# Kernel optimization log

Measured on AMD Instinct MI355X. Metric: run time of the kernel, lower is better.

## Reference

```python
import jax, jax.numpy as jnp
import numpy as np

T, B, H, V, L = 1024, 16, 1024, 100, 3


def setup_inputs() -> dict:
    key = jax.random.key(0)
    k_x, k_e, k_w, k_b = jax.random.split(key, 4)
    x = jax.random.randint(k_x, (T, B), 0, V)                      # [T, B] token ids
    emb = jax.random.normal(k_e, (V, H), dtype=jnp.float32) * 0.1  # embedding table
    # per-layer Linear(H, 3H): stacked weights/biases (all layers have in=out=H)
    W = jax.random.normal(k_w, (L, H, 3 * H), dtype=jnp.float32) * (1.0 / np.sqrt(H))
    b = jax.random.normal(k_b, (L, 3 * H), dtype=jnp.float32) * 0.01
    return {"x": x, "emb": emb, "W": W, "b": b}


def _qrnn_layer(h, W_l, b_l):
    # h: [T, B, H] -> gates [T, B, 3H]
    g = jnp.einsum("tbh,hk->tbk", h, W_l) + b_l
    z, f, o = jnp.split(g, 3, axis=-1)
    z = jnp.tanh(z)
    f = jax.nn.sigmoid(f)
    o = jax.nn.sigmoid(o)

    def step(c, zf):
        z_t, f_t = zf
        c = f_t * z_t + (1.0 - f_t) * c  # forget-mult recurrence
        return c, c

    c0 = jnp.zeros(h.shape[1:], dtype=h.dtype)  # hidden init is None -> zeros
    _, C = jax.lax.scan(step, c0, (z, f))       # C: [T, B, H]
    return o * C


def reference(x, emb, W, b):
    h = emb[x]  # [T, B, H]
    for l in range(L):
        h = _qrnn_layer(h, W[l], b[l])
    return h[:-1]  # drop last timestep, [T-1, B, H]
```

## Files before the change

### kernel.cpp

```cpp
#include <hip/hip_runtime.h>
#include <hip/hip_bf16.h>

#define T_DIM 1024
#define B_DIM 16
#define H_DIM 1024
#define L_DIM 3
#define M_DIM (T_DIM * B_DIM)
#define N_DIM (3 * H_DIM)
#define K_DIM H_DIM
#define NC 64
#define CS 16

typedef __bf16 bf16x8 __attribute__((ext_vector_type(8)));
typedef __bf16 bf16x4 __attribute__((ext_vector_type(4)));
typedef _Float16 half4 __attribute__((ext_vector_type(4)));
typedef float f32x4 __attribute__((ext_vector_type(4)));

__device__ __forceinline__ __bf16 f2bf(float f) {
    return (__bf16)__float2bfloat16(f);
}

__device__ __forceinline__ void async_cp16(const void* g, void* lds) {
    __builtin_amdgcn_global_load_lds(
        (__attribute__((address_space(1))) void*)g,
        (__attribute__((address_space(3))) void*)lds, 16, 0, 0);
}

#define TW_BLOCKS (32 * 96 * 3)
__global__ void prep_kernel(const float* __restrict__ W, __bf16* __restrict__ Wt,
                            const int* __restrict__ x, const float4* __restrict__ emb,
                            __bf16* __restrict__ h) {
    if (blockIdx.x < TW_BLOCKS) {
        __shared__ __bf16 tile[32][33];
        const int blk = blockIdx.x;
        const int l = blk / 3072;
        const int r2 = blk % 3072;
        const int n0 = (r2 / 32) * 32, k0 = (r2 % 32) * 32;
        const int tx = threadIdx.x & 31, ty = threadIdx.x >> 5;
        const float* Wl = W + (size_t)l * K_DIM * N_DIM;
        __bf16* Wtl = Wt + (size_t)l * N_DIM * K_DIM;
#pragma unroll
        for (int q = 0; q < 4; q++) {
            int k = ty + q * 8;
            tile[k][tx] = f2bf(Wl[(size_t)(k0 + k) * N_DIM + n0 + tx]);
        }
        __syncthreads();
#pragma unroll
        for (int q = 0; q < 4; q++) {
            int n = ty + q * 8;
            Wtl[(size_t)(n0 + n) * K_DIM + k0 + tx] = tile[tx][n];
        }
    } else {
        int i = (blockIdx.x - TW_BLOCKS) * 256 + threadIdx.x;
        int row = i >> 8;
        int j = i & 255;
        int idx = x[row];
        float4 v = emb[(size_t)idx * 256 + j];
        __bf16* dst = h + (size_t)row * H_DIM + j * 4;
        dst[0] = f2bf(v.x); dst[1] = f2bf(v.y); dst[2] = f2bf(v.z); dst[3] = f2bf(v.w);
    }
}

__global__ __launch_bounds__(512, 2) void gemm_gates(
    const __bf16* __restrict__ A,
    const __bf16* __restrict__ Wt,
    const float* __restrict__ bias,
    _Float16* __restrict__ Gz, _Float16* __restrict__ Gf, _Float16* __restrict__ Go) {
    __shared__ __align__(16) __bf16 As[4 * 8192];
    __shared__ __align__(16) __bf16 Bs[4 * 8192];

    const int tid = threadIdx.x;
    const int lane = tid & 63, wid = tid >> 6;
    const int lm = lane & 15, kg = lane >> 4;
    const int waveM = wid >> 2, waveN = wid & 3;

    const int orig = blockIdx.x;
    const int lin = (orig & 7) * 96 + (orig >> 3);
    const int bm = lin / 12, bn = lin % 12;

    const int sr = tid >> 2;
    const int sch = (tid & 3) ^ ((sr >> 1) & 3);
    const int ga0 = sr * K_DIM + sch * 8;
    const int ga1 = (sr + 128) * K_DIM + sch * 8;
    const int lo0 = tid * 8;
    const int lo1 = (512 + tid) * 8;

    const __bf16* Abase = A + (size_t)(bm * 256) * K_DIM;
    const __bf16* Bbase = Wt + (size_t)(bn * 256) * K_DIM;

    const int slot8 = (kg ^ ((lm >> 1) & 3)) * 8;
    const int a_off0 = (waveM * 128 + 0 * 16 + lm) * 32 + slot8;
    const int a_off1 = (waveM * 128 + 1 * 16 + lm) * 32 + slot8;
    const int a_off2 = (waveM * 128 + 2 * 16 + lm) * 32 + slot8;
    const int a_off3 = (waveM * 128 + 3 * 16 + lm) * 32 + slot8;
    const int b_off0 = (waveN * 64 + 0 * 16 + lm) * 32 + slot8;
    const int b_off1 = (waveN * 64 + 1 * 16 + lm) * 32 + slot8;
    const int b_off2 = (waveN * 64 + 2 * 16 + lm) * 32 + slot8;
    const int b_off3 = (waveN * 64 + 3 * 16 + lm) * 32 + slot8;

    f32x4 acc[8][4] = {};
    bf16x8 af0, af1, af2, af3;
    bf16x8 bf0 = {}, bf1 = {}, bf2 = {}, bf3 = {};

#define STAGE(ARR, GB, TILE, KH) { \
    const int tt_ = (TILE) & 15; \
    const int kc_ = tt_ * 64 + (KH) * 32; \
    __bf16* dst_ = (ARR) + ((tt_ & 1) * 2 + (KH)) * 8192; \
    async_cp16((GB) + kc_ + ga0, dst_ + lo0); \
    async_cp16((GB) + kc_ + ga1, dst_ + lo1); }

#define MF1(IA, J, AF, BF) \
    acc[IA][J] = __builtin_amdgcn_mfma_f32_16x16x32_bf16(AF, BF, acc[IA][J], 0, 0, 0);
#define MF4(IA, AF) MF1(IA, 0, AF, bf0) MF1(IA, 1, AF, bf1) MF1(IA, 2, AF, bf2) MF1(IA, 3, AF, bf3)

#define PHASE(BUF, KH, MQ, LB, STG, VM) { \
    const __bf16* rA_ = As + ((BUF) * 2 + (KH)) * 8192 + (MQ) * 2048; \
    if (LB) { \
        const __bf16* rB_ = Bs + ((BUF) * 2 + (KH)) * 8192; \
        bf0 = *(const bf16x8*)(rB_ + b_off0); \
        bf1 = *(const bf16x8*)(rB_ + b_off1); \
        bf2 = *(const bf16x8*)(rB_ + b_off2); \
        bf3 = *(const bf16x8*)(rB_ + b_off3); } \
    af0 = *(const bf16x8*)(rA_ + a_off0); \
    af1 = *(const bf16x8*)(rA_ + a_off1); \
    af2 = *(const bf16x8*)(rA_ + a_off2); \
    af3 = *(const bf16x8*)(rA_ + a_off3); \
    STG; \
    __builtin_amdgcn_s_setprio(1); \
    MF4((MQ) * 4 + 0, af0) MF4((MQ) * 4 + 1, af1) MF4((MQ) * 4 + 2, af2) MF4((MQ) * 4 + 3, af3) \
    __builtin_amdgcn_s_setprio(0); \
    if (VM) { asm volatile("s_waitcnt vmcnt(8)" ::: "memory"); } \
    __builtin_amdgcn_s_barrier(); \
    __builtin_amdgcn_sched_barrier(0); }

    STAGE(As, Abase, 0, 0) STAGE(Bs, Bbase, 0, 0)
    STAGE(As, Abase, 0, 1) STAGE(Bs, Bbase, 0, 1)
    STAGE(As, Abase, 1, 0) STAGE(Bs, Bbase, 1, 0)
    asm volatile("s_waitcnt vmcnt(8)" ::: "memory");
    __builtin_amdgcn_s_barrier();
    __builtin_amdgcn_sched_barrier(0);

#pragma unroll 1
    for (int t = 0; t < 16; t += 2) {
        PHASE(0, 0, 0, 1, STAGE(As, Abase, t + 1, 1), 0)
        PHASE(0, 0, 1, 0, STAGE(Bs, Bbase, t + 1, 1), 1)
        PHASE(0, 1, 0, 1, STAGE(As, Abase, t + 2, 0), 0)
        PHASE(0, 1, 1, 0, STAGE(Bs, Bbase, t + 2, 0), 1)
        PHASE(1, 0, 0, 1, STAGE(As, Abase, t + 2, 1), 0)
        PHASE(1, 0, 1, 0, STAGE(Bs, Bbase, t + 2, 1), 1)
        PHASE(1, 1, 0, 1, STAGE(As, Abase, t + 3, 0), 0)
        PHASE(1, 1, 1, 0, STAGE(Bs, Bbase, t + 3, 0), 1)
    }
    asm volatile("s_waitcnt vmcnt(0)" ::: "memory");

#undef PHASE
#undef MF4
#undef MF1
#undef STAGE

    const int plane = bn >> 2;
    _Float16* __restrict__ P = (plane == 0) ? Gz : (plane == 1) ? Gf : Go;
    const int colbase = (bn & 3) * 256 + waveN * 64;
    const int nb = bn * 256 + waveN * 64;
#pragma unroll
    for (int mq = 0; mq < 2; mq++) {
#pragma unroll
        for (int i = 0; i < 4; i++) {
#pragma unroll
            for (int j = 0; j < 4; j++) {
                int col = colbase + j * 16 + lm;
                float bv = bias[nb + j * 16 + lm];
#pragma unroll
                for (int r = 0; r < 4; r++) {
                    int mrow = bm * 256 + waveM * 128 + mq * 64 + i * 16 + kg * 4 + r;
                    float g = acc[mq * 4 + i][j][r] + bv;
                    float val;
                    if (plane == 0) {
                        float e = __expf(-2.0f * fabsf(g));
                        float rc = __builtin_amdgcn_rcpf(1.0f + e);
                        val = copysignf(fmaf(-2.0f * e, rc, 1.0f), g);
                    } else {
                        float e = __expf(-g);
                        val = __builtin_amdgcn_rcpf(1.0f + e);
                    }
                    P[(size_t)mrow * H_DIM + col] = (_Float16)val;
                }
            }
        }
    }
}

__global__ __launch_bounds__(256, 8) void scan_pass1(
    const _Float16* __restrict__ Gz, const _Float16* __restrict__ Gf,
    float* __restrict__ cA, float* __restrict__ cM) {
    int tidg = blockIdx.x * 256 + threadIdx.x;
    int ci = tidg >> 12;
    int chg = tidg & 4095;
    size_t base = (size_t)(ci * CS) * 16384 + (size_t)chg * 4;
    f32x4 Aacc = {0.f, 0.f, 0.f, 0.f};
    f32x4 Macc = {1.f, 1.f, 1.f, 1.f};
#pragma unroll
    for (int s = 0; s < CS; s++) {
        half4 z = *(const half4*)(Gz + base);
        half4 f = *(const half4*)(Gf + base);
#pragma unroll
        for (int k = 0; k < 4; k++) {
            float fk = (float)f[k], zk = (float)z[k];
            Aacc[k] = fk * zk + (1.f - fk) * Aacc[k];
            Macc[k] = (1.f - fk) * Macc[k];
        }
        base += 16384;
    }
    size_t idx = (size_t)ci * 16384 + (size_t)chg * 4;
    *(f32x4*)(cA + idx) = Aacc;
    *(f32x4*)(cM + idx) = Macc;
}

__global__ __launch_bounds__(256, 8) void scan_pass23(
    const _Float16* __restrict__ Gz, const _Float16* __restrict__ Gf,
    const _Float16* __restrict__ Go,
    const float* __restrict__ cA, const float* __restrict__ cM,
    __bf16* __restrict__ hdst, float* __restrict__ fdst, int is_last) {
    int tidg = blockIdx.x * 256 + threadIdx.x;
    int ci = tidg >> 12;
    int chg = tidg & 4095;
    f32x4 c = {0.f, 0.f, 0.f, 0.f};
    for (int cj = 0; cj < ci; cj++) {
        size_t jdx = (size_t)cj * 16384 + (size_t)chg * 4;
        f32x4 a = *(const f32x4*)(cA + jdx);
        f32x4 m = *(const f32x4*)(cM + jdx);
#pragma unroll
        for (int k = 0; k < 4; k++) c[k] = a[k] + m[k] * c[k];
    }
    size_t p = (size_t)(ci * CS) * 16384 + (size_t)chg * 4;
#pragma unroll
    for (int s = 0; s < CS; s++) {
        int t = ci * CS + s;
        half4 z = *(const half4*)(Gz + p);
        half4 f = *(const half4*)(Gf + p);
        half4 o = *(const half4*)(Go + p);
        f32x4 val;
#pragma unroll
        for (int k = 0; k < 4; k++) {
            float fk = (float)f[k];
            c[k] = fk * (float)z[k] + (1.f - fk) * c[k];
            val[k] = (float)o[k] * c[k];
        }
        if (is_last) {
            if (t < T_DIM - 1)
                *(f32x4*)(fdst + p) = val;
        } else {
            bf16x4 hv;
#pragma unroll
            for (int k = 0; k < 4; k++) hv[k] = f2bf(val[k]);
            *(bf16x4*)(hdst + p) = hv;
        }
        p += 16384;
    }
}

extern "C" void kernel_launch(void* const* d_in, const int* in_sizes, int n_in,
                              void* d_out, int out_size, void* d_ws, size_t ws_size,
                              hipStream_t stream) {
    const int* x = (const int*)d_in[0];
    const float* emb = (const float*)d_in[1];
    const float* W = (const float*)d_in[2];
    const float* b = (const float*)d_in[3];
    float* out = (float*)d_out;

    char* ws = (char*)d_ws;
    size_t need = (size_t)L_DIM * N_DIM * K_DIM * 2
                + (size_t)M_DIM * H_DIM * 2
                + 3ull * M_DIM * H_DIM * 2
                + 2ull * NC * 16384 * 4;
    if (ws_size < need) return;

    __bf16* Wt = (__bf16*)ws;     ws += (size_t)L_DIM * N_DIM * K_DIM * 2;
    __bf16* hbuf = (__bf16*)ws;   ws += (size_t)M_DIM * H_DIM * 2;
    _Float16* Gz = (_Float16*)ws; ws += (size_t)M_DIM * H_DIM * 2;
    _Float16* Gf = (_Float16*)ws; ws += (size_t)M_DIM * H_DIM * 2;
    _Float16* Go = (_Float16*)ws; ws += (size_t)M_DIM * H_DIM * 2;
    float* cA = (float*)ws;       ws += (size_t)NC * 16384 * 4;
    float* cM = (float*)ws;

    prep_kernel<<<TW_BLOCKS + 16384, 256, 0, stream>>>(W, Wt, x, (const float4*)emb, hbuf);

    for (int l = 0; l < L_DIM; l++) {
        gemm_gates<<<dim3(768), 512, 0, stream>>>(
            hbuf, Wt + (size_t)l * N_DIM * K_DIM, b + (size_t)l * N_DIM, Gz, Gf, Go);
        int last = (l == L_DIM - 1);
        scan_pass1<<<1024, 256, 0, stream>>>(Gz, Gf, cA, cM);
        scan_pass23<<<1024, 256, 0, stream>>>(Gz, Gf, Go, cA, cM, hbuf, out, last);
    }
}
```

Before: 564.9 us.

## Shrink GEMM tile to 128x256 with simple double-buffered K loop for occupancy

The gate GEMM block tile is halved in M (256 to 128), so the grid doubles to 1536 blocks. LDS use drops from 128 KB to 48 KB per block and the launch bounds ask for 4 blocks per CU. The elaborate 4-buffer, 8-phase software pipeline with partial vmcnt waits is replaced by a plain two-buffer loop over 32-wide K steps, which waits on vmcnt(0) every iteration. The aim is to hide latency through occupancy rather than explicit pipelining, at the cost of lower per-block operand reuse, more barriers and less overlap of global loads with MFMA work.

```diff
diff --git a/kernel.cpp b/kernel.cpp
--- a/kernel.cpp
+++ b/kernel.cpp
@@ -61,130 +61,117 @@
     }
 }
 
-__global__ __launch_bounds__(512, 2) void gemm_gates(
+__global__ __launch_bounds__(512, 4) void gemm_gates(
     const __bf16* __restrict__ A,
     const __bf16* __restrict__ Wt,
     const float* __restrict__ bias,
     _Float16* __restrict__ Gz, _Float16* __restrict__ Gf, _Float16* __restrict__ Go) {
-    __shared__ __align__(16) __bf16 As[4 * 8192];
-    __shared__ __align__(16) __bf16 Bs[4 * 8192];
+    __shared__ __align__(16) __bf16 As[2 * 4096];
+    __shared__ __align__(16) __bf16 Bs[2 * 8192];
 
     const int tid = threadIdx.x;
     const int lane = tid & 63, wid = tid >> 6;
     const int lm = lane & 15, kg = lane >> 4;
-    const int waveM = wid >> 2, waveN = wid & 3;
+    const int wm = wid >> 2, wn = wid & 3;
 
     const int orig = blockIdx.x;
-    const int lin = (orig & 7) * 96 + (orig >> 3);
+    const int lin = (orig & 7) * 192 + (orig >> 3);
     const int bm = lin / 12, bn = lin % 12;
 
-    const int sr = tid >> 2;
-    const int sch = (tid & 3) ^ ((sr >> 1) & 3);
-    const int ga0 = sr * K_DIM + sch * 8;
-    const int ga1 = (sr + 128) * K_DIM + sch * 8;
-    const int lo0 = tid * 8;
-    const int lo1 = (512 + tid) * 8;
-
-    const __bf16* Abase = A + (size_t)(bm * 256) * K_DIM;
+    const int arow = tid >> 2;
+    const int asch = (tid & 3) ^ ((arow >> 1) & 3);
+    const int gaA = arow * K_DIM + asch * 8;
+    const int loA = tid * 8;
+    const int brow0 = tid >> 2, brow1 = (512 + tid) >> 2;
+    const int bsch0 = (tid & 3) ^ ((brow0 >> 1) & 3);
+    const int bsch1 = (tid & 3) ^ ((brow1 >> 1) & 3);
+    const int gaB0 = brow0 * K_DIM + bsch0 * 8;
+    const int gaB1 = brow1 * K_DIM + bsch1 * 8;
+    const int loB0 = tid * 8;
+    const int loB1 = (512 + tid) * 8;
+
+    const __bf16* Abase = A + (size_t)(bm * 128) * K_DIM;
     const __bf16* Bbase = Wt + (size_t)(bn * 256) * K_DIM;
 
     const int slot8 = (kg ^ ((lm >> 1) & 3)) * 8;
-    const int a_off0 = (waveM * 128 + 0 * 16 + lm) * 32 + slot8;
-    const int a_off1 = (waveM * 128 + 1 * 16 + lm) * 32 + slot8;
-    const int a_off2 = (waveM * 128 + 2 * 16 + lm) * 32 + slot8;
-    const int a_off3 = (waveM * 128 + 3 * 16 + lm) * 32 + slot8;
-    const int b_off0 = (waveN * 64 + 0 * 16 + lm) * 32 + slot8;
-    const int b_off1 = (waveN * 64 + 1 * 16 + lm) * 32 + slot8;
-    const int b_off2 = (waveN * 64 + 2 * 16 + lm) * 32 + slot8;
-    const int b_off3 = (waveN * 64 + 3 * 16 + lm) * 32 + slot8;
-
-    f32x4 acc[8][4] = {};
-    bf16x8 af0, af1, af2, af3;
-    bf16x8 bf0 = {}, bf1 = {}, bf2 = {}, bf3 = {};
-
-#define STAGE(ARR, GB, TILE, KH) { \
-    const int tt_ = (TILE) & 15; \
-    const int kc_ = tt_ * 64 + (KH) * 32; \
-    __bf16* dst_ = (ARR) + ((tt_ & 1) * 2 + (KH)) * 8192; \
-    async_cp16((GB) + kc_ + ga0, dst_ + lo0); \
-    async_cp16((GB) + kc_ + ga1, dst_ + lo1); }
-
-#define MF1(IA, J, AF, BF) \
-    acc[IA][J] = __builtin_amdgcn_mfma_f32_16x16x32_bf16(AF, BF, acc[IA][J], 0, 0, 0);
-#define MF4(IA, AF) MF1(IA, 0, AF, bf0) MF1(IA, 1, AF, bf1) MF1(IA, 2, AF, bf2) MF1(IA, 3, AF, bf3)
-
-#define PHASE(BUF, KH, MQ, LB, STG, VM) { \
-    const __bf16* rA_ = As + ((BUF) * 2 + (KH)) * 8192 + (MQ) * 2048; \
-    if (LB) { \
-        const __bf16* rB_ = Bs + ((BUF) * 2 + (KH)) * 8192; \
-        bf0 = *(const bf16x8*)(rB_ + b_off0); \
-        bf1 = *(const bf16x8*)(rB_ + b_off1); \
-        bf2 = *(const bf16x8*)(rB_ + b_off2); \
-        bf3 = *(const bf16x8*)(rB_ + b_off3); } \
-    af0 = *(const bf16x8*)(rA_ + a_off0); \
-    af1 = *(const bf16x8*)(rA_ + a_off1); \
-    af2 = *(const bf16x8*)(rA_ + a_off2); \
-    af3 = *(const bf16x8*)(rA_ + a_off3); \
-    STG; \
-    __builtin_amdgcn_s_setprio(1); \
-    MF4((MQ) * 4 + 0, af0) MF4((MQ) * 4 + 1, af1) MF4((MQ) * 4 + 2, af2) MF4((MQ) * 4 + 3, af3) \
-    __builtin_amdgcn_s_setprio(0); \
-    if (VM) { asm volatile("s_waitcnt vmcnt(8)" ::: "memory"); } \
-    __builtin_amdgcn_s_barrier(); \
-    __builtin_amdgcn_sched_barrier(0); }
-
-    STAGE(As, Abase, 0, 0) STAGE(Bs, Bbase, 0, 0)
-    STAGE(As, Abase, 0, 1) STAGE(Bs, Bbase, 0, 1)
-    STAGE(As, Abase, 1, 0) STAGE(Bs, Bbase, 1, 0)
-    asm volatile("s_waitcnt vmcnt(8)" ::: "memory");
+    const int a_off0 = (wm * 64 + 0 * 16 + lm) * 32 + slot8;
+    const int a_off1 = (wm * 64 + 1 * 16 + lm) * 32 + slot8;
+    const int a_off2 = (wm * 64 + 2 * 16 + lm) * 32 + slot8;
+    const int a_off3 = (wm * 64 + 3 * 16 + lm) * 32 + slot8;
+    const int b_off0 = (wn * 64 + 0 * 16 + lm) * 32 + slot8;
+    const int b_off1 = (wn * 64 + 1 * 16 + lm) * 32 + slot8;
+    const int b_off2 = (wn * 64 + 2 * 16 + lm) * 32 + slot8;
+    const int b_off3 = (wn * 64 + 3 * 16 + lm) * 32 + slot8;
+
+    f32x4 acc[4][4] = {};
+
+#define STAGE(TN) { \
+    const int kc_ = (TN) * 32; \
+    const int nb_ = (TN) & 1; \
+    async_cp16(Abase + kc_ + gaA, As + nb_ * 4096 + loA); \
+    async_cp16(Bbase + kc_ + gaB0, Bs + nb_ * 8192 + loB0); \
+    async_cp16(Bbase + kc_ + gaB1, Bs + nb_ * 8192 + loB1); }
+
+    STAGE(0)
+    asm volatile("s_waitcnt vmcnt(0)" ::: "memory");
     __builtin_amdgcn_s_barrier();
     __builtin_amdgcn_sched_barrier(0);
 
 #pragma unroll 1
-    for (int t = 0; t < 16; t += 2) {
-        PHASE(0, 0, 0, 1, STAGE(As, Abase, t + 1, 1), 0)
-        PHASE(0, 0, 1, 0, STAGE(Bs, Bbase, t + 1, 1), 1)
-        PHASE(0, 1, 0, 1, STAGE(As, Abase, t + 2, 0), 0)
-        PHASE(0, 1, 1, 0, STAGE(Bs, Bbase, t + 2, 0), 1)
-        PHASE(1, 0, 0, 1, STAGE(As, Abase, t + 2, 1), 0)
-        PHASE(1, 0, 1, 0, STAGE(Bs, Bbase, t + 2, 1), 1)
-        PHASE(1, 1, 0, 1, STAGE(As, Abase, t + 3, 0), 0)
-        PHASE(1, 1, 1, 0, STAGE(Bs, Bbase, t + 3, 0), 1)
-    }
-    asm volatile("s_waitcnt vmcnt(0)" ::: "memory");
-
-#undef PHASE
-#undef MF4
-#undef MF1
+    for (int t = 0; t < 32; ++t) {
+        const int cur = t & 1;
+        const __bf16* rA = As + cur * 4096;
+        const __bf16* rB = Bs + cur * 8192;
+        bf16x8 bf0 = *(const bf16x8*)(rB + b_off0);
+        bf16x8 bf1 = *(const bf16x8*)(rB + b_off1);
+        bf16x8 bf2 = *(const bf16x8*)(rB + b_off2);
+        bf16x8 bf3 = *(const bf16x8*)(rB + b_off3);
+        bf16x8 af0 = *(const bf16x8*)(rA + a_off0);
+        bf16x8 af1 = *(const bf16x8*)(rA + a_off1);
+        bf16x8 af2 = *(const bf16x8*)(rA + a_off2);
+        bf16x8 af3 = *(const bf16x8*)(rA + a_off3);
+        const int tn = (t + 1) & 31;
+        STAGE(tn)
+        __builtin_amdgcn_s_setprio(1);
+#define MFJ(I, AF) \
+        acc[I][0] = __builtin_amdgcn_mfma_f32_16x16x32_bf16(AF, bf0, acc[I][0], 0, 0, 0); \
+        acc[I][1] = __builtin_amdgcn_mfma_f32_16x16x32_bf16(AF, bf1, acc[I][1], 0, 0, 0); \
+        acc[I][2] = __builtin_amdgcn_mfma_f32_16x16x32_bf16(AF, bf2, acc[I][2], 0, 0, 0); \
+        acc[I][3] = __builtin_amdgcn_mfma_f32_16x16x32_bf16(AF, bf3, acc[I][3], 0, 0, 0);
+        MFJ(0, af0) MFJ(1, af1) MFJ(2, af2) MFJ(3, af3)
+#undef MFJ
+        __builtin_amdgcn_s_setprio(0);
+        asm volatile("s_waitcnt vmcnt(0)" ::: "memory");
+        __builtin_amdgcn_s_barrier();
+        __builtin_amdgcn_sched_barrier(0);
+    }
+
 #undef STAGE
 
     const int plane = bn >> 2;
     _Float16* __restrict__ P = (plane == 0) ? Gz : (plane == 1) ? Gf : Go;
-    const int colbase = (bn & 3) * 256 + waveN * 64;
-    const int nb = bn * 256 + waveN * 64;
-#pragma unroll
-    for (int mq = 0; mq < 2; mq++) {
-#pragma unroll
-        for (int i = 0; i < 4; i++) {
-#pragma unroll
-            for (int j = 0; j < 4; j++) {
-                int col = colbase + j * 16 + lm;
-                float bv = bias[nb + j * 16 + lm];
-#pragma unroll
-                for (int r = 0; r < 4; r++) {
-                    int mrow = bm * 256 + waveM * 128 + mq * 64 + i * 16 + kg * 4 + r;
-                    float g = acc[mq * 4 + i][j][r] + bv;
-                    float val;
-                    if (plane == 0) {
-                        float e = __expf(-2.0f * fabsf(g));
-                        float rc = __builtin_amdgcn_rcpf(1.0f + e);
-                        val = copysignf(fmaf(-2.0f * e, rc, 1.0f), g);
-                    } else {
-                        float e = __expf(-g);
-                        val = __builtin_amdgcn_rcpf(1.0f + e);
-                    }
-                    P[(size_t)mrow * H_DIM + col] = (_Float16)val;
+    const int colbase = (bn & 3) * 256 + wn * 64;
+    const int nb = bn * 256 + wn * 64;
+#pragma unroll
+    for (int i = 0; i < 4; i++) {
+#pragma unroll
+        for (int j = 0; j < 4; j++) {
+            int col = colbase + j * 16 + lm;
+            float bv = bias[nb + j * 16 + lm];
+#pragma unroll
+            for (int r = 0; r < 4; r++) {
+                int mrow = bm * 128 + wm * 64 + i * 16 + kg * 4 + r;
+                float g = acc[i][j][r] + bv;
+                float val;
+                if (plane == 0) {
+                    float e = __expf(-2.0f * fabsf(g));
+                    float rc = __builtin_amdgcn_rcpf(1.0f + e);
+                    val = copysignf(fmaf(-2.0f * e, rc, 1.0f), g);
+                } else {
+                    float e = __expf(-g);
+                    val = __builtin_amdgcn_rcpf(1.0f + e);
                 }
+                P[(size_t)mrow * H_DIM + col] = (_Float16)val;
             }
         }
     }
@@ -286,7 +273,7 @@
     prep_kernel<<<TW_BLOCKS + 16384, 256, 0, stream>>>(W, Wt, x, (const float4*)emb, hbuf);
 
     for (int l = 0; l < L_DIM; l++) {
-        gemm_gates<<<dim3(768), 512, 0, stream>>>(
+        gemm_gates<<<dim3(1536), 512, 0, stream>>>(
             hbuf, Wt + (size_t)l * N_DIM * K_DIM, b + (size_t)l * N_DIM, Gz, Gf, Go);
         int last = (l == L_DIM - 1);
         scan_pass1<<<1024, 256, 0, stream>>>(Gz, Gf, cA, cM);
```

After: 574.8 us. No clear change (+1.7%).
